# Optimization experiments

Hardware: AMD Instinct MI355X
Metric: run time of the kernel (lower is better)

Reference implementation:

```python
import jax, jax.numpy as jnp
import numpy as np

VOCAB = 65
N_EMBED = 384
BLOCK = 256
N_HEAD = 6
HEAD_SIZE = 4  # forward uses sa_heads = MultiHeadAttention(4), NOT the Block stack
B, T = 128, 256


def setup_inputs() -> dict:
    key = jax.random.key(0)
    ks = jax.random.split(key, 16)
    s = lambda *sh: 0.02
    inp = {
        "idx": jax.random.randint(ks[0], (B, T), 0, VOCAB),
        "targets": jax.random.randint(ks[1], (B, T), 0, VOCAB),
        "tok_emb": jax.random.normal(ks[2], (VOCAB, N_EMBED), jnp.float32) * 0.02,
        "pos_emb": jax.random.normal(ks[3], (BLOCK, N_EMBED), jnp.float32) * 0.02,
        "Wq": jax.random.normal(ks[4], (N_HEAD, N_EMBED, HEAD_SIZE), jnp.float32) * 0.05,
        "Wk": jax.random.normal(ks[5], (N_HEAD, N_EMBED, HEAD_SIZE), jnp.float32) * 0.05,
        "Wv": jax.random.normal(ks[6], (N_HEAD, N_EMBED, HEAD_SIZE), jnp.float32) * 0.05,
        "Wproj": jax.random.normal(ks[7], (N_HEAD * HEAD_SIZE, N_EMBED), jnp.float32) * 0.05,
        "bproj": jnp.zeros((N_EMBED,), jnp.float32),
        "W1": jax.random.normal(ks[8], (N_EMBED, 4 * N_EMBED), jnp.float32) * 0.02,
        "b1": jnp.zeros((4 * N_EMBED,), jnp.float32),
        "W2": jax.random.normal(ks[9], (4 * N_EMBED, N_EMBED), jnp.float32) * 0.02,
        "b2": jnp.zeros((N_EMBED,), jnp.float32),
        "Wlm": jax.random.normal(ks[10], (N_EMBED, VOCAB), jnp.float32) * 0.02,
        "blm": jnp.zeros((VOCAB,), jnp.float32),
    }
    return inp


def _forward(idx, targets, tok_emb, pos_emb, Wq, Wk, Wv, Wproj, bproj, W1, b1, W2, b2, Wlm, blm):
    Bb, Tt = idx.shape
    x = tok_emb[idx] + pos_emb[:Tt]  # [B,T,C]
    # multi-head attention (manual, causal). NOTE: source scales by n_embed**-0.5 (C of input), not head_size.
    q = jnp.einsum("btc,hcd->bhtd", x, Wq)
    k = jnp.einsum("btc,hcd->bhtd", x, Wk)
    v = jnp.einsum("btc,hcd->bhtd", x, Wv)
    scores = jnp.einsum("bhtd,bhsd->bhts", q, k) * (N_EMBED ** -0.5)
    causal = jnp.tril(jnp.ones((Tt, Tt), bool))
    scores = jnp.where(causal, scores, -jnp.inf)
    w = jax.nn.softmax(scores, axis=-1)  # dropout = identity in eval
    attn = jnp.einsum("bhts,bhsd->bhtd", w, v)
    attn = attn.transpose(0, 2, 1, 3).reshape(Bb, Tt, N_HEAD * HEAD_SIZE)
    x = attn @ Wproj + bproj
    # feed-forward
    x = jax.nn.relu(x @ W1 + b1) @ W2 + b2
    logits = x @ Wlm + blm  # [B,T,V]
    logits_flat = logits.reshape(Bb * Tt, VOCAB)
    t_flat = targets.reshape(Bb * Tt)
    logp = jax.nn.log_softmax(logits_flat, axis=-1)
    loss = -jnp.mean(jnp.take_along_axis(logp, t_flat[:, None], axis=1))
    return logits_flat, loss


def reference(idx, targets, tok_emb, pos_emb, Wq, Wk, Wv, Wproj, bproj, W1, b1, W2, b2, Wlm, blm):
    return _forward(idx, targets, tok_emb, pos_emb, Wq, Wk, Wv, Wproj, bproj, W1, b1, W2, b2, Wlm, blm)
```

## Files before the change

### kernel.cpp

```cpp
#include <hip/hip_runtime.h>
#include <hip/hip_bf16.h>
#include <math.h>

typedef __hip_bfloat16 bf16;
typedef __attribute__((ext_vector_type(8))) short bf16x8;
typedef __attribute__((ext_vector_type(4))) float f32x4;
typedef __attribute__((ext_vector_type(8))) int i32x8;
typedef __attribute__((ext_vector_type(4))) int i32x4;
typedef unsigned char u8;
typedef unsigned int u32;

#define T_SEQ   256
#define C_EMB   384
#define NH      6
#define HS      4
#define NB      128
#define NTOK    (NB * T_SEQ)
#define VOC     65
#define FFDIM   1536
#define QKVW    72
#define PROJK   32
#define XROWS   (VOC * T_SEQ)

#define X2_SCALE    128.0f
#define W1_SCALE    128.0f
#define FF1_DESCALE (1.0f / (128.0f * 128.0f))
#define H1_SCALE    512.0f
#define W2_SCALE    128.0f
#define FF2_DESCALE (1.0f / (512.0f * 128.0f))

__device__ __forceinline__ float b2f(bf16 x) { return __bfloat162float(x); }
__device__ __forceinline__ bf16  f2b(float x) { return __float2bfloat16(x); }
__device__ __forceinline__ short f2s(float x) { bf16 b = __float2bfloat16(x); return *reinterpret_cast<short*>(&b); }
__device__ __forceinline__ u8 f2fp8(float x) {
    return (u8)(__builtin_amdgcn_cvt_pk_fp8_f32(x, x, 0, false) & 0xff);
}
__device__ __forceinline__ u32 pk4fp8(const float* w) {
    int p = __builtin_amdgcn_cvt_pk_fp8_f32(w[0], w[1], 0, false);
    p = __builtin_amdgcn_cvt_pk_fp8_f32(w[2], w[3], p, true);
    return (u32)p;
}

__device__ __forceinline__ void glds16(const void* g, void* l) {
    __builtin_amdgcn_global_load_lds((const __attribute__((address_space(1))) void*)g,
                                     (__attribute__((address_space(3))) void*)l, 16, 0, 0);
}

__global__ void pack_all_kernel(const float* __restrict__ Wq, const float* __restrict__ Wk,
                                const float* __restrict__ Wv, const float* __restrict__ Wlm,
                                const float* __restrict__ Wproj,
                                const float* __restrict__ W1, const float* __restrict__ W2,
                                const float* __restrict__ tok_emb, const float* __restrict__ pos_emb,
                                bf16* __restrict__ WqkvT, bf16* __restrict__ WlmT,
                                bf16* __restrict__ WprojT, u8* __restrict__ W1f8,
                                u8* __restrict__ W2f8, bf16* __restrict__ xtab) {
    int blk = blockIdx.x;
    if (blk < 128) {
        int n = blk;
        for (int c = threadIdx.x; c < C_EMB; c += 256) {
            float v = 0.f;
            if (n < QKVW) {
                int sel = n / 24, r = n % 24, h = r >> 2, d = r & 3;
                const float* W = (sel == 0) ? Wq : (sel == 1) ? Wk : Wv;
                v = W[(h * C_EMB + c) * HS + d];
            }
            WqkvT[(size_t)n * C_EMB + c] = f2b(v);
        }
    } else if (blk < 256) {
        int n = blk - 128;
        for (int c = threadIdx.x; c < C_EMB; c += 256)
            WlmT[(size_t)n * C_EMB + c] = f2b(n < VOC ? Wlm[(size_t)c * VOC + n] : 0.f);
    } else if (blk < 640) {
        int n = blk - 256;
        int k = threadIdx.x;
        if (k < PROJK)
            WprojT[(size_t)n * PROJK + k] = f2b(k < 24 ? Wproj[(size_t)k * C_EMB + n] : 0.f);
    } else if (blk < 640 + FFDIM) {
        int n = blk - 640;
        for (int k = threadIdx.x; k < C_EMB; k += 256)
            W1f8[(size_t)n * C_EMB + k] = f2fp8(W1[(size_t)k * FFDIM + n] * W1_SCALE);
    } else if (blk < 640 + FFDIM + C_EMB) {
        int n = blk - 640 - FFDIM;
        for (int k = threadIdx.x; k < FFDIM; k += 256)
            W2f8[(size_t)n * FFDIM + k] = f2fp8(W2[(size_t)k * C_EMB + n] * W2_SCALE);
    } else {
        int base = (blk - (640 + FFDIM + C_EMB)) * 4;
        for (int r = 0; r < 4; ++r) {
            int row = base + r;
            int id = row >> 8, t = row & 255;
            const float* te = tok_emb + (size_t)id * C_EMB;
            const float* pe = pos_emb + (size_t)t * C_EMB;
            bf16* dst = xtab + (size_t)row * C_EMB;
            for (int c = threadIdx.x; c < C_EMB; c += 256)
                dst[c] = f2b(te[c] + pe[c]);
        }
    }
}

__global__ __launch_bounds__(512)
void qkv_gather_kernel(const int* __restrict__ idx, const bf16* __restrict__ xtab,
                       const bf16* __restrict__ Bt, float* __restrict__ outf) {
    __shared__ short As[128][32];
    __shared__ short Bs[128][32];
    __shared__ int rowid[128];
    int tid = threadIdx.x, lane = tid & 63, wave = tid >> 6;
    int bm = blockIdx.x * 128;
    int wm = (wave & 1) * 64, wn = (wave >> 1) * 32;
    int lrow = lane & 15, khalf = lane >> 4;
    if (tid < 128) { int token = bm + tid; rowid[tid] = idx[token] * T_SEQ + (token & (T_SEQ - 1)); }
    __syncthreads();

    int row = tid >> 2;
    int i0 = (tid & 3) * 16;
    int selem = ((i0 - ((row >> 1) & 3) * 16) & 63) >> 1;
    long ga = (long)rowid[row] * C_EMB;
    int arot = ((lrow >> 1) & 3) * 16;
    int roff = ((khalf * 16 + arot) & 63) >> 1;

    f32x4 acc[4][2] = {};
    for (int k0 = 0; k0 < C_EMB; k0 += 32) {
        glds16(xtab + ga + k0 + selem,                (short*)As + (size_t)tid * 8);
        glds16(Bt + (size_t)row * C_EMB + k0 + selem, (short*)Bs + (size_t)tid * 8);
        __syncthreads();

        bf16x8 af[4], bff[2];
        #pragma unroll
        for (int i = 0; i < 4; ++i)
            af[i] = *(const bf16x8*)&As[wm + i * 16 + lrow][roff];
        #pragma unroll
        for (int i = 0; i < 2; ++i)
            bff[i] = *(const bf16x8*)&Bs[wn + i * 16 + lrow][roff];
        #pragma unroll
        for (int mi = 0; mi < 4; ++mi)
            #pragma unroll
            for (int ni = 0; ni < 2; ++ni)
                acc[mi][ni] = __builtin_amdgcn_mfma_f32_16x16x32_bf16(af[mi], bff[ni], acc[mi][ni], 0, 0, 0);
        __syncthreads();
    }

    #pragma unroll
    for (int ni = 0; ni < 2; ++ni) {
        int col = wn + ni * 16 + lrow;
        if (col >= QKVW) continue;
        #pragma unroll
        for (int mi = 0; mi < 4; ++mi) {
            int orow = bm + wm + mi * 16 + khalf * 4;
            #pragma unroll
            for (int r = 0; r < 4; ++r)
                outf[(size_t)(orow + r) * QKVW + col] = acc[mi][ni][r];
        }
    }
}

__global__ void attn_kernel(const float* __restrict__ qkv,
                            bf16* __restrict__ attnT) {
    int bh = blockIdx.x;
    int b = bh / NH, h = bh % NH;
    int t = threadIdx.x;
    __shared__ float ks[T_SEQ][HS];
    __shared__ float vs[T_SEQ][HS];
    const float* base = qkv + (size_t)(b * T_SEQ) * QKVW;
    #pragma unroll
    for (int d = 0; d < HS; ++d) {
        ks[t][d] = base[t * QKVW + 24 + h * HS + d];
        vs[t][d] = base[t * QKVW + 48 + h * HS + d];
    }
    __syncthreads();
    const float* qp = base + t * QKVW + h * HS;
    float q0 = qp[0], q1 = qp[1], q2 = qp[2], q3 = qp[3];
    const float scale = 0.05103103630798288f;
    float m = -1e30f, sum = 0.f, o0 = 0.f, o1 = 0.f, o2 = 0.f, o3 = 0.f;
    for (int s = 0; s <= t; ++s) {
        float sc = (q0 * ks[s][0] + q1 * ks[s][1] + q2 * ks[s][2] + q3 * ks[s][3]) * scale;
        float mn = fmaxf(m, sc);
        float alpha = __expf(m - mn);
        float p = __expf(sc - mn);
        sum = sum * alpha + p;
        o0 = o0 * alpha + p * vs[s][0];
        o1 = o1 * alpha + p * vs[s][1];
        o2 = o2 * alpha + p * vs[s][2];
        o3 = o3 * alpha + p * vs[s][3];
        m = mn;
    }
    float inv = 1.f / sum;
    bf16* out = attnT + (size_t)(b * T_SEQ + t) * PROJK + h * HS;
    out[0] = f2b(o0 * inv); out[1] = f2b(o1 * inv); out[2] = f2b(o2 * inv); out[3] = f2b(o3 * inv);
    if (h == 0) {
        bf16* pad = attnT + (size_t)(b * T_SEQ + t) * PROJK + 24;
        *(uint4*)pad = uint4{0, 0, 0, 0};
    }
}

__global__ __launch_bounds__(256)
void gemm_mfma32_kernel(const bf16* __restrict__ A, const bf16* __restrict__ Bt,
                        const float* __restrict__ bias,
                        u8* __restrict__ outf8, float oscale,
                        int M, int K, int Nout) {
    __shared__ short As[128][32];
    __shared__ short Bs[128][32];
    int tid  = threadIdx.x;
    int lane = tid & 63;
    int wave = tid >> 6;
    int bm = blockIdx.y * 128;
    int bn = blockIdx.x * 128;
    int wm = (wave & 1) * 64;
    int wn = (wave >> 1) * 64;
    int lrow  = lane & 15;
    int khalf = lane >> 4;
    int arot = ((lrow >> 1) & 3) * 16;
    int roff = ((khalf * 16 + arot) & 63) >> 1;

    f32x4 acc[4][4] = {};
    for (int k0 = 0; k0 < K; k0 += 32) {
        #pragma unroll
        for (int h = 0; h < 2; ++h) {
            int c = tid + h * 256;
            int row = c >> 2;
            int i0 = (c & 3) * 16;
            int selem = ((i0 - ((row >> 1) & 3) * 16) & 63) >> 1;
            glds16(A  + (size_t)(bm + row) * K + k0 + selem, (short*)As + (size_t)c * 8);
            glds16(Bt + (size_t)(bn + row) * K + k0 + selem, (short*)Bs + (size_t)c * 8);
        }
        __syncthreads();

        bf16x8 af[4], bff[4];
        #pragma unroll
        for (int i = 0; i < 4; ++i) {
            af[i]  = *(const bf16x8*)&As[wm + i * 16 + lrow][roff];
            bff[i] = *(const bf16x8*)&Bs[wn + i * 16 + lrow][roff];
        }
        #pragma unroll
        for (int mi = 0; mi < 4; ++mi)
            #pragma unroll
            for (int ni = 0; ni < 4; ++ni)
                acc[mi][ni] = __builtin_amdgcn_mfma_f32_16x16x32_bf16(af[mi], bff[ni], acc[mi][ni], 0, 0, 0);
        __syncthreads();
    }

    #pragma unroll
    for (int ni = 0; ni < 4; ++ni) {
        int col = bn + wn + ni * 16 + lrow;
        float bv = bias[col];
        #pragma unroll
        for (int mi = 0; mi < 4; ++mi) {
            int row = bm + wm + mi * 16 + khalf * 4;
            float w[4];
            #pragma unroll
            for (int r = 0; r < 4; ++r) w[r] = (acc[mi][ni][r] + bv) * oscale;
            int p01 = __builtin_amdgcn_cvt_pk_fp8_f32(w[0], w[1], 0, false);
            int p23 = __builtin_amdgcn_cvt_pk_fp8_f32(w[2], w[3], 0, false);
            outf8[(size_t)(row + 0) * Nout + col] = (u8)(p01 & 0xff);
            outf8[(size_t)(row + 1) * Nout + col] = (u8)((p01 >> 8) & 0xff);
            outf8[(size_t)(row + 2) * Nout + col] = (u8)(p23 & 0xff);
            outf8[(size_t)(row + 3) * Nout + col] = (u8)((p23 >> 8) & 0xff);
        }
    }
}

__global__ __launch_bounds__(512)
void gemm_fp8_kernel(const u8* __restrict__ A, const u8* __restrict__ Bt,
                     const float* __restrict__ bias,
                     bf16* __restrict__ outb, u8* __restrict__ outf8,
                     float descale, float oscale,
                     int M, int K, int Nout, int NT, int relu) {
    __shared__ u8 smem[32768];
    u8* As = smem;
    u8* Bs = smem + 16384;
    int lin  = blockIdx.x;
    int xcd  = lin & 7;
    int loc  = lin >> 3;
    int nt   = loc % NT;
    int mloc = loc / NT;
    int MPX  = (M / 128) >> 3;
    int bm = (xcd * MPX + mloc) * 128;
    int bn = nt * 128;

    int tid  = threadIdx.x;
    int lane = tid & 63;
    int wave = tid >> 6;
    int wm = (wave & 1) * 64;
    int wn = (wave >> 1) * 32;
    int lrow  = lane & 15;
    int khalf = lane >> 4;

    f32x4 acc[4][2] = {};
    int r0 = tid >> 3;
    int i0 = (tid & 7) * 16;
    int s0 = (i0 - (r0 & 7) * 16) & 127;
    int arot = (lrow & 7) * 16;
    int off0 = (khalf * 32 + arot) & 127;
    int off1 = (off0 + 16) & 127;

    for (int k0 = 0; k0 < K; k0 += 128) {
        const u8* Ag = A  + (size_t)(bm + r0) * K + k0 + s0;
        const u8* Bg = Bt + (size_t)(bn + r0) * K + k0 + s0;
        glds16(Ag,                  As + (size_t)tid * 16);
        glds16(Ag + (size_t)64 * K, As + 8192 + (size_t)tid * 16);
        glds16(Bg,                  Bs + (size_t)tid * 16);
        glds16(Bg + (size_t)64 * K, Bs + 8192 + (size_t)tid * 16);
        __syncthreads();

        i32x8 a[4], b[2];
        #pragma unroll
        for (int i = 0; i < 4; ++i) {
            const u8* rp = As + (size_t)(wm + i * 16 + lrow) * 128;
            i32x4 lo = *(const i32x4*)(rp + off0);
            i32x4 hi = *(const i32x4*)(rp + off1);
            a[i][0]=lo[0]; a[i][1]=lo[1]; a[i][2]=lo[2]; a[i][3]=lo[3];
            a[i][4]=hi[0]; a[i][5]=hi[1]; a[i][6]=hi[2]; a[i][7]=hi[3];
        }
        #pragma unroll
        for (int i = 0; i < 2; ++i) {
            const u8* rp = Bs + (size_t)(wn + i * 16 + lrow) * 128;
            i32x4 lo = *(const i32x4*)(rp + off0);
            i32x4 hi = *(const i32x4*)(rp + off1);
            b[i][0]=lo[0]; b[i][1]=lo[1]; b[i][2]=lo[2]; b[i][3]=lo[3];
            b[i][4]=hi[0]; b[i][5]=hi[1]; b[i][6]=hi[2]; b[i][7]=hi[3];
        }
        #pragma unroll
        for (int mi = 0; mi < 4; ++mi)
            #pragma unroll
            for (int ni = 0; ni < 2; ++ni)
                acc[mi][ni] = __builtin_amdgcn_mfma_scale_f32_16x16x128_f8f6f4(
                    b[ni], a[mi], acc[mi][ni], 0, 0,
                    0, 0x7f7f7f7f, 0, 0x7f7f7f7f);
        __syncthreads();
    }

    if (outf8) {
        #pragma unroll
        for (int mi = 0; mi < 4; ++mi) {
            int m = wm + mi * 16 + lrow;
            #pragma unroll
            for (int ni = 0; ni < 2; ++ni) {
                int n0 = wn + ni * 16 + khalf * 4;
                float4 bv = *(const float4*)(bias + bn + n0);
                float w[4];
                w[0] = acc[mi][ni][0] * descale + bv.x;
                w[1] = acc[mi][ni][1] * descale + bv.y;
                w[2] = acc[mi][ni][2] * descale + bv.z;
                w[3] = acc[mi][ni][3] * descale + bv.w;
                if (relu) {
                    w[0] = fmaxf(w[0], 0.f); w[1] = fmaxf(w[1], 0.f);
                    w[2] = fmaxf(w[2], 0.f); w[3] = fmaxf(w[3], 0.f);
                }
                w[0] *= oscale; w[1] *= oscale; w[2] *= oscale; w[3] *= oscale;
                *(u32*)&smem[(size_t)m * 128 + ((n0 + (m & 7) * 16) & 127)] = pk4fp8(w);
            }
        }
        __syncthreads();
        #pragma unroll
        for (int p = 0; p < 2; ++p) {
            int c = tid + p * 512;
            int row = c >> 3;
            int g0 = (c & 7) * 16;
            uint4 v = *(const uint4*)&smem[(size_t)row * 128 + ((g0 + (row & 7) * 16) & 127)];
            *(uint4*)&outf8[(size_t)(bm + row) * Nout + bn + g0] = v;
        }
    } else {
        short* Es = (short*)smem;
        #pragma unroll
        for (int mi = 0; mi < 4; ++mi) {
            int m = wm + mi * 16 + lrow;
            #pragma unroll
            for (int ni = 0; ni < 2; ++ni) {
                int n0 = wn + ni * 16 + khalf * 4;
                float4 bv = *(const float4*)(bias + bn + n0);
                union { short s[4]; uint2 u; } pk;
                pk.s[0] = f2s(acc[mi][ni][0] * descale + bv.x);
                pk.s[1] = f2s(acc[mi][ni][1] * descale + bv.y);
                pk.s[2] = f2s(acc[mi][ni][2] * descale + bv.z);
                pk.s[3] = f2s(acc[mi][ni][3] * descale + bv.w);
                *(uint2*)&Es[(size_t)m * 128 + ((n0 + (m & 7) * 8) & 127)] = pk.u;
            }
        }
        __syncthreads();
        #pragma unroll
        for (int p = 0; p < 4; ++p) {
            int c = tid + p * 512;
            int row = c >> 4;
            int g0 = (c & 15) * 16;
            uint4 v = *(const uint4*)&smem[(size_t)row * 256 + ((g0 + (row & 7) * 16) & 255)];
            *(uint4*)((u8*)outb + ((size_t)(bm + row) * Nout + bn) * 2 + g0) = v;
        }
    }
}

__global__ __launch_bounds__(512)
void lm_loss_kernel(const bf16* __restrict__ A, const bf16* __restrict__ Bt,
                    const float* __restrict__ bias, const int* __restrict__ targets,
                    float* __restrict__ outf, float* __restrict__ lossbuf,
                    int M, int K) {
    __shared__ short As[128][32];
    __shared__ short Bs[128][32];
    __shared__ float Ls[128][66];
    int tid  = threadIdx.x;
    int lane = tid & 63;
    int wave = tid >> 6;
    int bm = blockIdx.x * 128;
    int wm = (wave & 1) * 64;
    int wn = (wave >> 1) * 32;
    int lrow  = lane & 15;
    int khalf = lane >> 4;

    int row = tid >> 2;
    int i0 = (tid & 3) * 16;
    int selem = ((i0 - ((row >> 1) & 3) * 16) & 63) >> 1;
    int arot = ((lrow >> 1) & 3) * 16;
    int roff = ((khalf * 16 + arot) & 63) >> 1;

    f32x4 acc[4][2] = {};
    for (int k0 = 0; k0 < K; k0 += 32) {
        glds16(A  + (size_t)(bm + row) * K + k0 + selem, (short*)As + (size_t)tid * 8);
        glds16(Bt + (size_t)row * K + k0 + selem,        (short*)Bs + (size_t)tid * 8);
        __syncthreads();

        bf16x8 af[4], bff[2];
        #pragma unroll
        for (int i = 0; i < 4; ++i)
            af[i] = *(const bf16x8*)&As[wm + i * 16 + lrow][roff];
        #pragma unroll
        for (int i = 0; i < 2; ++i)
            bff[i] = *(const bf16x8*)&Bs[wn + i * 16 + lrow][roff];
        #pragma unroll
        for (int mi = 0; mi < 4; ++mi)
            #pragma unroll
            for (int ni = 0; ni < 2; ++ni)
                acc[mi][ni] = __builtin_amdgcn_mfma_f32_16x16x32_bf16(af[mi], bff[ni], acc[mi][ni], 0, 0, 0);
        __syncthreads();
    }

    #pragma unroll
    for (int ni = 0; ni < 2; ++ni) {
        int col = wn + ni * 16 + lrow;
        if (col >= VOC) continue;
        float bv = bias[col];
        #pragma unroll
        for (int mi = 0; mi < 4; ++mi) {
            int lr = wm + mi * 16 + khalf * 4;
            #pragma unroll
            for (int r = 0; r < 4; ++r) {
                float v = acc[mi][ni][r] + bv;
                outf[(size_t)(bm + lr + r) * VOC + col] = v;
                Ls[lr + r][col] = v;
            }
        }
    }
    __syncthreads();

    if (tid < 128) {
        int token = bm + tid;
        int tgt = targets[token];
        float m = -1e30f, s = 0.f;
        #pragma unroll 8
        for (int c = 0; c < VOC; ++c) {
            float v = Ls[tid][c];
            float mn = fmaxf(m, v);
            s = s * __expf(m - mn) + __expf(v - mn);
            m = mn;
        }
        lossbuf[token] = m + logf(s) - Ls[tid][tgt];
    }
}

__global__ void loss_reduce_kernel(const float* __restrict__ lossbuf, float* __restrict__ out_loss) {
    __shared__ float red[256];
    int tid = threadIdx.x;
    float s = 0.f;
    for (int i = tid; i < NTOK; i += 256) s += lossbuf[i];
    red[tid] = s; __syncthreads();
    for (int st = 128; st > 0; st >>= 1) { if (tid < st) red[tid] += red[tid + st]; __syncthreads(); }
    if (tid == 0) out_loss[0] = red[0] / (float)NTOK;
}

extern "C" void kernel_launch(void* const* d_in, const int* in_sizes, int n_in,
                              void* d_out, int out_size, void* d_ws, size_t ws_size,
                              hipStream_t stream) {
    const int*   idx     = (const int*)  d_in[0];
    const int*   targets = (const int*)  d_in[1];
    const float* tok_emb = (const float*)d_in[2];
    const float* pos_emb = (const float*)d_in[3];
    const float* Wq      = (const float*)d_in[4];
    const float* Wk      = (const float*)d_in[5];
    const float* Wv      = (const float*)d_in[6];
    const float* Wproj   = (const float*)d_in[7];
    const float* bproj   = (const float*)d_in[8];
    const float* W1      = (const float*)d_in[9];
    const float* b1      = (const float*)d_in[10];
    const float* W2      = (const float*)d_in[11];
    const float* b2      = (const float*)d_in[12];
    const float* Wlm     = (const float*)d_in[13];
    const float* blm     = (const float*)d_in[14];

    char* ws = (char*)d_ws;
    bf16*  WprojT = (bf16*) (ws + 0);
    float* qkvbuf = (float*)(ws + 25165824);
    bf16*  attnT  = (bf16*) (ws + 34603008);
    bf16*  xtab   = (bf16*) (ws + 37748736);
    u8*    h1f8   = (u8*)   (ws + 62914560);
    u8*    x2f8   = (u8*)   (ws + 113246208);
    bf16*  x3     = (bf16*) (ws + 163577856);
    float* lossbuf= (float*)(ws + 188743680);
    u8*    W1f8   = (u8*)   (ws + 188874752);
    u8*    W2f8   = (u8*)   (ws + 190054400);
    bf16*  WqkvT  = (bf16*) (ws + 191234048);
    bf16*  WlmT   = (bf16*) (ws + 191332352);

    float* out_logits = (float*)d_out;
    float* out_loss   = out_logits + (size_t)NTOK * VOC;

    pack_all_kernel<<<640 + FFDIM + C_EMB + XROWS / 4, 256, 0, stream>>>(
        Wq, Wk, Wv, Wlm, Wproj, W1, W2, tok_emb, pos_emb,
        WqkvT, WlmT, WprojT, W1f8, W2f8, xtab);

    qkv_gather_kernel<<<NTOK / 128, 512, 0, stream>>>(idx, xtab, WqkvT, qkvbuf);
    attn_kernel<<<NB * NH, T_SEQ, 0, stream>>>(qkvbuf, attnT);

    gemm_mfma32_kernel<<<dim3(C_EMB / 128, NTOK / 128), 256, 0, stream>>>(attnT, WprojT, bproj,
                                                                          x2f8, X2_SCALE,
                                                                          NTOK, PROJK, C_EMB);
    gemm_fp8_kernel<<<(NTOK / 128) * (FFDIM / 128), 512, 0, stream>>>(x2f8, W1f8, b1,
                                                                      nullptr, h1f8,
                                                                      FF1_DESCALE, H1_SCALE,
                                                                      NTOK, C_EMB, FFDIM, FFDIM / 128, 1);
    gemm_fp8_kernel<<<(NTOK / 128) * (C_EMB / 128), 512, 0, stream>>>(h1f8, W2f8, b2,
                                                                      x3, nullptr,
                                                                      FF2_DESCALE, 1.0f,
                                                                      NTOK, FFDIM, C_EMB, C_EMB / 128, 0);
    lm_loss_kernel<<<NTOK / 128, 512, 0, stream>>>(x3, WlmT, blm, targets,
                                                   out_logits, lossbuf, NTOK, C_EMB);

    loss_reduce_kernel<<<1, 256, 0, stream>>>(lossbuf, out_loss);
}
```

Measured before the change: 261.0 us.

## Enlarge fp8 GEMM tile to 256 rows and fuse loss reduction via atomics

The fp8 FFN GEMM now computes a 256x128 tile per block. Each of the 8 waves owns 32 rows across all 128 columns, which cuts redundant B loads and raises MFMA work per LDS load. Shared memory grows to 48KB and the bf16 epilogue is staged in two halves. Separately, the final loss reduction kernel is removed: each lm_loss block reduces its tokens and atomically adds into a global accumulator, and a completion counter lets the last block write the mean. This makes the loss summation order nondeterministic and raises LDS use, which may lower occupancy.

```diff
diff --git a/kernel.cpp b/kernel.cpp
--- a/kernel.cpp
+++ b/kernel.cpp
@@ -46,6 +46,15 @@
                                      (__attribute__((address_space(3))) void*)l, 16, 0, 0);
 }
 
+__device__ __forceinline__ i32x8 ld_pair(const u8* rp, int off0, int off1) {
+    i32x4 lo = *(const i32x4*)(rp + off0);
+    i32x4 hi = *(const i32x4*)(rp + off1);
+    i32x8 r;
+    r[0]=lo[0]; r[1]=lo[1]; r[2]=lo[2]; r[3]=lo[3];
+    r[4]=hi[0]; r[5]=hi[1]; r[6]=hi[2]; r[7]=hi[3];
+    return r;
+}
+
 __global__ void pack_all_kernel(const float* __restrict__ Wq, const float* __restrict__ Wk,
                                 const float* __restrict__ Wv, const float* __restrict__ Wlm,
                                 const float* __restrict__ Wproj,
@@ -53,8 +62,10 @@
                                 const float* __restrict__ tok_emb, const float* __restrict__ pos_emb,
                                 bf16* __restrict__ WqkvT, bf16* __restrict__ WlmT,
                                 bf16* __restrict__ WprojT, u8* __restrict__ W1f8,
-                                u8* __restrict__ W2f8, bf16* __restrict__ xtab) {
+                                u8* __restrict__ W2f8, bf16* __restrict__ xtab,
+                                float* __restrict__ lossbuf) {
     int blk = blockIdx.x;
+    if (blk == 0 && threadIdx.x == 0) { lossbuf[0] = 0.f; ((int*)lossbuf)[1] = 0; }
     if (blk < 128) {
         int n = blk;
         for (int c = threadIdx.x; c < C_EMB; c += 256) {
@@ -263,27 +274,26 @@
                      bf16* __restrict__ outb, u8* __restrict__ outf8,
                      float descale, float oscale,
                      int M, int K, int Nout, int NT, int relu) {
-    __shared__ u8 smem[32768];
+    __shared__ u8 smem[49152];
     u8* As = smem;
-    u8* Bs = smem + 16384;
+    u8* Bs = smem + 32768;
     int lin  = blockIdx.x;
     int xcd  = lin & 7;
     int loc  = lin >> 3;
     int nt   = loc % NT;
     int mloc = loc / NT;
-    int MPX  = (M / 128) >> 3;
-    int bm = (xcd * MPX + mloc) * 128;
+    int MPX  = (M / 256) >> 3;
+    int bm = (xcd * MPX + mloc) * 256;
     int bn = nt * 128;
 
     int tid  = threadIdx.x;
     int lane = tid & 63;
     int wave = tid >> 6;
-    int wm = (wave & 1) * 64;
-    int wn = (wave >> 1) * 32;
+    int wm = wave * 32;
     int lrow  = lane & 15;
     int khalf = lane >> 4;
 
-    f32x4 acc[4][2] = {};
+    f32x4 acc[2][8] = {};
     int r0 = tid >> 3;
     int i0 = (tid & 7) * 16;
     int s0 = (i0 - (r0 & 7) * 16) & 127;
@@ -292,48 +302,42 @@
     int off1 = (off0 + 16) & 127;
 
     for (int k0 = 0; k0 < K; k0 += 128) {
-        const u8* Ag = A  + (size_t)(bm + r0) * K + k0 + s0;
-        const u8* Bg = Bt + (size_t)(bn + r0) * K + k0 + s0;
-        glds16(Ag,                  As + (size_t)tid * 16);
-        glds16(Ag + (size_t)64 * K, As + 8192 + (size_t)tid * 16);
-        glds16(Bg,                  Bs + (size_t)tid * 16);
-        glds16(Bg + (size_t)64 * K, Bs + 8192 + (size_t)tid * 16);
-        __syncthreads();
-
-        i32x8 a[4], b[2];
-        #pragma unroll
-        for (int i = 0; i < 4; ++i) {
-            const u8* rp = As + (size_t)(wm + i * 16 + lrow) * 128;
-            i32x4 lo = *(const i32x4*)(rp + off0);
-            i32x4 hi = *(const i32x4*)(rp + off1);
-            a[i][0]=lo[0]; a[i][1]=lo[1]; a[i][2]=lo[2]; a[i][3]=lo[3];
-            a[i][4]=hi[0]; a[i][5]=hi[1]; a[i][6]=hi[2]; a[i][7]=hi[3];
-        }
-        #pragma unroll
-        for (int i = 0; i < 2; ++i) {
-            const u8* rp = Bs + (size_t)(wn + i * 16 + lrow) * 128;
-            i32x4 lo = *(const i32x4*)(rp + off0);
-            i32x4 hi = *(const i32x4*)(rp + off1);
-            b[i][0]=lo[0]; b[i][1]=lo[1]; b[i][2]=lo[2]; b[i][3]=lo[3];
-            b[i][4]=hi[0]; b[i][5]=hi[1]; b[i][6]=hi[2]; b[i][7]=hi[3];
-        }
-        #pragma unroll
-        for (int mi = 0; mi < 4; ++mi)
-            #pragma unroll
-            for (int ni = 0; ni < 2; ++ni)
-                acc[mi][ni] = __builtin_amdgcn_mfma_scale_f32_16x16x128_f8f6f4(
-                    b[ni], a[mi], acc[mi][ni], 0, 0,
-                    0, 0x7f7f7f7f, 0, 0x7f7f7f7f);
+        #pragma unroll
+        for (int g = 0; g < 4; ++g)
+            glds16(A + (size_t)(bm + r0 + g * 64) * K + k0 + s0, As + (size_t)(tid + g * 512) * 16);
+        #pragma unroll
+        for (int g = 0; g < 2; ++g)
+            glds16(Bt + (size_t)(bn + r0 + g * 64) * K + k0 + s0, Bs + (size_t)(tid + g * 512) * 16);
+        __syncthreads();
+
+        i32x8 a[2];
+        #pragma unroll
+        for (int mi = 0; mi < 2; ++mi)
+            a[mi] = ld_pair(As + (size_t)(wm + mi * 16 + lrow) * 128, off0, off1);
+        #pragma unroll
+        for (int hf = 0; hf < 2; ++hf) {
+            i32x8 b[4];
+            #pragma unroll
+            for (int j = 0; j < 4; ++j)
+                b[j] = ld_pair(Bs + (size_t)((hf * 4 + j) * 16 + lrow) * 128, off0, off1);
+            #pragma unroll
+            for (int mi = 0; mi < 2; ++mi)
+                #pragma unroll
+                for (int j = 0; j < 4; ++j)
+                    acc[mi][hf * 4 + j] = __builtin_amdgcn_mfma_scale_f32_16x16x128_f8f6f4(
+                        b[j], a[mi], acc[mi][hf * 4 + j], 0, 0,
+                        0, 0x7f7f7f7f, 0, 0x7f7f7f7f);
+        }
         __syncthreads();
     }
 
     if (outf8) {
         #pragma unroll
-        for (int mi = 0; mi < 4; ++mi) {
+        for (int mi = 0; mi < 2; ++mi) {
             int m = wm + mi * 16 + lrow;
             #pragma unroll
-            for (int ni = 0; ni < 2; ++ni) {
-                int n0 = wn + ni * 16 + khalf * 4;
+            for (int ni = 0; ni < 8; ++ni) {
+                int n0 = ni * 16 + khalf * 4;
                 float4 bv = *(const float4*)(bias + bn + n0);
                 float w[4];
                 w[0] = acc[mi][ni][0] * descale + bv.x;
@@ -350,7 +354,7 @@
         }
         __syncthreads();
         #pragma unroll
-        for (int p = 0; p < 2; ++p) {
+        for (int p = 0; p < 4; ++p) {
             int c = tid + p * 512;
             int row = c >> 3;
             int g0 = (c & 7) * 16;
@@ -358,30 +362,36 @@
             *(uint4*)&outf8[(size_t)(bm + row) * Nout + bn + g0] = v;
         }
     } else {
-        short* Es = (short*)smem;
-        #pragma unroll
-        for (int mi = 0; mi < 4; ++mi) {
-            int m = wm + mi * 16 + lrow;
-            #pragma unroll
-            for (int ni = 0; ni < 2; ++ni) {
-                int n0 = wn + ni * 16 + khalf * 4;
-                float4 bv = *(const float4*)(bias + bn + n0);
-                union { short s[4]; uint2 u; } pk;
-                pk.s[0] = f2s(acc[mi][ni][0] * descale + bv.x);
-                pk.s[1] = f2s(acc[mi][ni][1] * descale + bv.y);
-                pk.s[2] = f2s(acc[mi][ni][2] * descale + bv.z);
-                pk.s[3] = f2s(acc[mi][ni][3] * descale + bv.w);
-                *(uint2*)&Es[(size_t)m * 128 + ((n0 + (m & 7) * 8) & 127)] = pk.u;
+        #pragma unroll
+        for (int p = 0; p < 2; ++p) {
+            if ((wave >> 2) == p) {
+                #pragma unroll
+                for (int mi = 0; mi < 2; ++mi) {
+                    int m = wm + mi * 16 + lrow;
+                    int ml = m - p * 128;
+                    #pragma unroll
+                    for (int ni = 0; ni < 8; ++ni) {
+                        int n0 = ni * 16 + khalf * 4;
+                        float4 bv = *(const float4*)(bias + bn + n0);
+                        union { short s[4]; uint2 u; } pk;
+                        pk.s[0] = f2s(acc[mi][ni][0] * descale + bv.x);
+                        pk.s[1] = f2s(acc[mi][ni][1] * descale + bv.y);
+                        pk.s[2] = f2s(acc[mi][ni][2] * descale + bv.z);
+                        pk.s[3] = f2s(acc[mi][ni][3] * descale + bv.w);
+                        *(uint2*)&smem[(size_t)ml * 256 + ((n0 * 2 + (ml & 7) * 16) & 255)] = pk.u;
+                    }
+                }
             }
-        }
-        __syncthreads();
-        #pragma unroll
-        for (int p = 0; p < 4; ++p) {
-            int c = tid + p * 512;
-            int row = c >> 4;
-            int g0 = (c & 15) * 16;
-            uint4 v = *(const uint4*)&smem[(size_t)row * 256 + ((g0 + (row & 7) * 16) & 255)];
-            *(uint4*)((u8*)outb + ((size_t)(bm + row) * Nout + bn) * 2 + g0) = v;
+            __syncthreads();
+            #pragma unroll
+            for (int p2 = 0; p2 < 4; ++p2) {
+                int c = tid + p2 * 512;
+                int row = c >> 4;
+                int g0 = (c & 15) * 16;
+                uint4 v = *(const uint4*)&smem[(size_t)row * 256 + ((g0 + (row & 7) * 16) & 255)];
+                *(uint4*)((u8*)outb + ((size_t)(bm + p * 128 + row) * Nout + bn) * 2 + g0) = v;
+            }
+            __syncthreads();
         }
     }
 }
@@ -390,10 +400,11 @@
 void lm_loss_kernel(const bf16* __restrict__ A, const bf16* __restrict__ Bt,
                     const float* __restrict__ bias, const int* __restrict__ targets,
                     float* __restrict__ outf, float* __restrict__ lossbuf,
-                    int M, int K) {
+                    float* __restrict__ out_loss, int M, int K) {
     __shared__ short As[128][32];
     __shared__ short Bs[128][32];
     __shared__ float Ls[128][66];
+    __shared__ float red[128];
     int tid  = threadIdx.x;
     int lane = tid & 63;
     int wave = tid >> 6;
@@ -459,18 +470,24 @@
             s = s * __expf(m - mn) + __expf(v - mn);
             m = mn;
         }
-        lossbuf[token] = m + logf(s) - Ls[tid][tgt];
-    }
-}
-
-__global__ void loss_reduce_kernel(const float* __restrict__ lossbuf, float* __restrict__ out_loss) {
-    __shared__ float red[256];
-    int tid = threadIdx.x;
-    float s = 0.f;
-    for (int i = tid; i < NTOK; i += 256) s += lossbuf[i];
-    red[tid] = s; __syncthreads();
-    for (int st = 128; st > 0; st >>= 1) { if (tid < st) red[tid] += red[tid + st]; __syncthreads(); }
-    if (tid == 0) out_loss[0] = red[0] / (float)NTOK;
+        red[tid] = m + logf(s) - Ls[tid][tgt];
+    }
+    __syncthreads();
+    if (tid < 64) {
+        float s = red[tid] + red[tid + 64];
+        #pragma unroll
+        for (int off = 32; off > 0; off >>= 1) s += __shfl_xor(s, off);
+        if (tid == 0) {
+            atomicAdd(&lossbuf[0], s);
+            __threadfence();
+            int done = atomicAdd(&((int*)lossbuf)[1], 1);
+            if (done == (NTOK / 128) - 1) {
+                __threadfence();
+                float total = atomicAdd(&lossbuf[0], 0.0f);
+                out_loss[0] = total / (float)NTOK;
+            }
+        }
+    }
 }
 
 extern "C" void kernel_launch(void* const* d_in, const int* in_sizes, int n_in,
@@ -511,7 +528,7 @@
 
     pack_all_kernel<<<640 + FFDIM + C_EMB + XROWS / 4, 256, 0, stream>>>(
         Wq, Wk, Wv, Wlm, Wproj, W1, W2, tok_emb, pos_emb,
-        WqkvT, WlmT, WprojT, W1f8, W2f8, xtab);
+        WqkvT, WlmT, WprojT, W1f8, W2f8, xtab, lossbuf);
 
     qkv_gather_kernel<<<NTOK / 128, 512, 0, stream>>>(idx, xtab, WqkvT, qkvbuf);
     attn_kernel<<<NB * NH, T_SEQ, 0, stream>>>(qkvbuf, attnT);
@@ -519,16 +536,14 @@
     gemm_mfma32_kernel<<<dim3(C_EMB / 128, NTOK / 128), 256, 0, stream>>>(attnT, WprojT, bproj,
                                                                           x2f8, X2_SCALE,
                                                                           NTOK, PROJK, C_EMB);
-    gemm_fp8_kernel<<<(NTOK / 128) * (FFDIM / 128), 512, 0, stream>>>(x2f8, W1f8, b1,
+    gemm_fp8_kernel<<<(NTOK / 256) * (FFDIM / 128), 512, 0, stream>>>(x2f8, W1f8, b1,
                                                                       nullptr, h1f8,
                                                                       FF1_DESCALE, H1_SCALE,
                                                                       NTOK, C_EMB, FFDIM, FFDIM / 128, 1);
-    gemm_fp8_kernel<<<(NTOK / 128) * (C_EMB / 128), 512, 0, stream>>>(h1f8, W2f8, b2,
+    gemm_fp8_kernel<<<(NTOK / 256) * (C_EMB / 128), 512, 0, stream>>>(h1f8, W2f8, b2,
                                                                       x3, nullptr,
                                                                       FF2_DESCALE, 1.0f,
                                                                       NTOK, FFDIM, C_EMB, C_EMB / 128, 0);
     lm_loss_kernel<<<NTOK / 128, 512, 0, stream>>>(x3, WlmT, blm, targets,
-                                                   out_logits, lossbuf, NTOK, C_EMB);
-
-    loss_reduce_kernel<<<1, 256, 0, stream>>>(lossbuf, out_loss);
-}
+                                                   out_logits, lossbuf, out_loss, NTOK, C_EMB);
+}
```

Measured after the change: 255.5 us. 1.02x faster.

## Load FP8 GEMM B operand directly from global and fuse loss reduction via atomics

Applied to the files above, without the earlier changes.

In the FP8 GEMM, the weight (B) tile is no longer staged through shared memory. Each wave reads its B fragments straight from global memory into registers, while the A tile still goes through LDS with swizzled direct loads. Separately, the final loss reduction kernel is removed: each lm_loss block reduces its 128 per-token losses in shared memory and adds the sum atomically, and the last block to finish writes the mean. This saves a kernel launch and halves LDS traffic, but the direct B reads may be less coalesced and the float atomics make the summation order nondeterministic.

```diff
diff --git a/kernel.cpp b/kernel.cpp
--- a/kernel.cpp
+++ b/kernel.cpp
@@ -46,6 +46,15 @@
                                      (__attribute__((address_space(3))) void*)l, 16, 0, 0);
 }
 
+__device__ __forceinline__ i32x8 ld_pair(const u8* rp, int off0, int off1) {
+    i32x4 lo = *(const i32x4*)(rp + off0);
+    i32x4 hi = *(const i32x4*)(rp + off1);
+    i32x8 r;
+    r[0]=lo[0]; r[1]=lo[1]; r[2]=lo[2]; r[3]=lo[3];
+    r[4]=hi[0]; r[5]=hi[1]; r[6]=hi[2]; r[7]=hi[3];
+    return r;
+}
+
 __global__ void pack_all_kernel(const float* __restrict__ Wq, const float* __restrict__ Wk,
                                 const float* __restrict__ Wv, const float* __restrict__ Wlm,
                                 const float* __restrict__ Wproj,
@@ -53,8 +62,10 @@
                                 const float* __restrict__ tok_emb, const float* __restrict__ pos_emb,
                                 bf16* __restrict__ WqkvT, bf16* __restrict__ WlmT,
                                 bf16* __restrict__ WprojT, u8* __restrict__ W1f8,
-                                u8* __restrict__ W2f8, bf16* __restrict__ xtab) {
+                                u8* __restrict__ W2f8, bf16* __restrict__ xtab,
+                                float* __restrict__ lossbuf) {
     int blk = blockIdx.x;
+    if (blk == 0 && threadIdx.x == 0) { lossbuf[0] = 0.f; ((int*)lossbuf)[1] = 0; }
     if (blk < 128) {
         int n = blk;
         for (int c = threadIdx.x; c < C_EMB; c += 256) {
@@ -265,7 +276,6 @@
                      int M, int K, int Nout, int NT, int relu) {
     __shared__ u8 smem[32768];
     u8* As = smem;
-    u8* Bs = smem + 16384;
     int lin  = blockIdx.x;
     int xcd  = lin & 7;
     int loc  = lin >> 3;
@@ -284,39 +294,34 @@
     int khalf = lane >> 4;
 
     f32x4 acc[4][2] = {};
-    int r0 = tid >> 3;
-    int i0 = (tid & 7) * 16;
-    int s0 = (i0 - (r0 & 7) * 16) & 127;
     int arot = (lrow & 7) * 16;
     int off0 = (khalf * 32 + arot) & 127;
     int off1 = (off0 + 16) & 127;
 
     for (int k0 = 0; k0 < K; k0 += 128) {
-        const u8* Ag = A  + (size_t)(bm + r0) * K + k0 + s0;
-        const u8* Bg = Bt + (size_t)(bn + r0) * K + k0 + s0;
-        glds16(Ag,                  As + (size_t)tid * 16);
-        glds16(Ag + (size_t)64 * K, As + 8192 + (size_t)tid * 16);
-        glds16(Bg,                  Bs + (size_t)tid * 16);
-        glds16(Bg + (size_t)64 * K, Bs + 8192 + (size_t)tid * 16);
-        __syncthreads();
-
-        i32x8 a[4], b[2];
-        #pragma unroll
-        for (int i = 0; i < 4; ++i) {
-            const u8* rp = As + (size_t)(wm + i * 16 + lrow) * 128;
-            i32x4 lo = *(const i32x4*)(rp + off0);
-            i32x4 hi = *(const i32x4*)(rp + off1);
-            a[i][0]=lo[0]; a[i][1]=lo[1]; a[i][2]=lo[2]; a[i][3]=lo[3];
-            a[i][4]=hi[0]; a[i][5]=hi[1]; a[i][6]=hi[2]; a[i][7]=hi[3];
-        }
+        #pragma unroll
+        for (int g = 0; g < 2; ++g) {
+            int c = tid + g * 512;
+            int row = c >> 3;
+            int i0 = (c & 7) * 16;
+            int s0 = (i0 - (row & 7) * 16) & 127;
+            glds16(A + (size_t)(bm + row) * K + k0 + s0, As + (size_t)c * 16);
+        }
+        i32x8 b[2];
         #pragma unroll
         for (int i = 0; i < 2; ++i) {
-            const u8* rp = Bs + (size_t)(wn + i * 16 + lrow) * 128;
-            i32x4 lo = *(const i32x4*)(rp + off0);
-            i32x4 hi = *(const i32x4*)(rp + off1);
+            const u8* rp = Bt + (size_t)(bn + wn + i * 16 + lrow) * K + k0 + khalf * 32;
+            i32x4 lo = *(const i32x4*)rp;
+            i32x4 hi = *(const i32x4*)(rp + 16);
             b[i][0]=lo[0]; b[i][1]=lo[1]; b[i][2]=lo[2]; b[i][3]=lo[3];
             b[i][4]=hi[0]; b[i][5]=hi[1]; b[i][6]=hi[2]; b[i][7]=hi[3];
         }
+        __syncthreads();
+
+        i32x8 a[4];
+        #pragma unroll
+        for (int i = 0; i < 4; ++i)
+            a[i] = ld_pair(As + (size_t)(wm + i * 16 + lrow) * 128, off0, off1);
         #pragma unroll
         for (int mi = 0; mi < 4; ++mi)
             #pragma unroll
@@ -390,10 +395,11 @@
 void lm_loss_kernel(const bf16* __restrict__ A, const bf16* __restrict__ Bt,
                     const float* __restrict__ bias, const int* __restrict__ targets,
                     float* __restrict__ outf, float* __restrict__ lossbuf,
-                    int M, int K) {
+                    float* __restrict__ out_loss, int M, int K) {
     __shared__ short As[128][32];
     __shared__ short Bs[128][32];
     __shared__ float Ls[128][66];
+    __shared__ float red[128];
     int tid  = threadIdx.x;
     int lane = tid & 63;
     int wave = tid >> 6;
@@ -459,18 +465,24 @@
             s = s * __expf(m - mn) + __expf(v - mn);
             m = mn;
         }
-        lossbuf[token] = m + logf(s) - Ls[tid][tgt];
-    }
-}
-
-__global__ void loss_reduce_kernel(const float* __restrict__ lossbuf, float* __restrict__ out_loss) {
-    __shared__ float red[256];
-    int tid = threadIdx.x;
-    float s = 0.f;
-    for (int i = tid; i < NTOK; i += 256) s += lossbuf[i];
-    red[tid] = s; __syncthreads();
-    for (int st = 128; st > 0; st >>= 1) { if (tid < st) red[tid] += red[tid + st]; __syncthreads(); }
-    if (tid == 0) out_loss[0] = red[0] / (float)NTOK;
+        red[tid] = m + logf(s) - Ls[tid][tgt];
+    }
+    __syncthreads();
+    if (tid < 64) {
+        float s = red[tid] + red[tid + 64];
+        #pragma unroll
+        for (int off = 32; off > 0; off >>= 1) s += __shfl_xor(s, off);
+        if (tid == 0) {
+            atomicAdd(&lossbuf[0], s);
+            __threadfence();
+            int done = atomicAdd(&((int*)lossbuf)[1], 1);
+            if (done == (NTOK / 128) - 1) {
+                __threadfence();
+                float total = atomicAdd(&lossbuf[0], 0.0f);
+                out_loss[0] = total / (float)NTOK;
+            }
+        }
+    }
 }
 
 extern "C" void kernel_launch(void* const* d_in, const int* in_sizes, int n_in,
@@ -511,7 +523,7 @@
 
     pack_all_kernel<<<640 + FFDIM + C_EMB + XROWS / 4, 256, 0, stream>>>(
         Wq, Wk, Wv, Wlm, Wproj, W1, W2, tok_emb, pos_emb,
-        WqkvT, WlmT, WprojT, W1f8, W2f8, xtab);
+        WqkvT, WlmT, WprojT, W1f8, W2f8, xtab, lossbuf);
 
     qkv_gather_kernel<<<NTOK / 128, 512, 0, stream>>>(idx, xtab, WqkvT, qkvbuf);
     attn_kernel<<<NB * NH, T_SEQ, 0, stream>>>(qkvbuf, attnT);
@@ -528,7 +540,5 @@
                                                                       FF2_DESCALE, 1.0f,
                                                                       NTOK, FFDIM, C_EMB, C_EMB / 128, 0);
     lm_loss_kernel<<<NTOK / 128, 512, 0, stream>>>(x3, WlmT, blm, targets,
-                                                   out_logits, lossbuf, NTOK, C_EMB);
-
-    loss_reduce_kernel<<<1, 256, 0, stream>>>(lossbuf, out_loss);
-}
+                                                   out_logits, lossbuf, out_loss, NTOK, C_EMB);
+}
```

Result: no change. 261.9 us (+0.3%).
